# Performance work log

Measured on AMD Instinct MI355X. Metric: run time of the kernel, lower is better.

The kernel has to match this reference:

```python
import jax, jax.numpy as jnp
import numpy as np
import math

EPS = 1e-9
NORM = 1.0 / math.sqrt(20.0)  # num_neighbours=20 default


def _mixing(x1, x2, B, W, b):
    # nn.Bilinear (no bias): x_bi[n,k] = sum_ij x1[n,i] B[k,i,j] x2[n,j]
    x_bi = jnp.einsum('ni,kij->nkj', x1, B)
    x_bi = jnp.einsum('nkj,nj->nk', x_bi, x2)
    x = jnp.concatenate([x1, x2, x_bi], axis=-1)
    return x @ W.T + b


def _rowstd(x):
    # torch.std default: unbiased (ddof=1)
    return jnp.std(x, axis=1, ddof=1, keepdims=True)


def setup_inputs() -> dict:
    key = jax.random.key(0)
    N, E = 100000, 2000000
    DN, DE, DA_N, DA_E = 32, 32, 3, 1
    ks = jax.random.split(key, 24)

    def nrm(k, shape, fan_in):
        return jax.random.normal(k, shape, dtype=jnp.float32) / np.sqrt(fan_in)

    inp = {
        'xn': jax.random.normal(ks[0], (N, DN), dtype=jnp.float32),
        'xn_attr': jax.random.normal(ks[1], (N, DA_N), dtype=jnp.float32),
        'xe_attr': jax.random.normal(ks[2], (E, DA_E), dtype=jnp.float32),
        'xe_src': jax.random.randint(ks[3], (E,), 0, N),
        'xe_dst': jax.random.randint(ks[4], (E,), 0, N),
        # fc1: Linear(1, xe_dim); fc2: Linear(1, xn_dim)
        'W_fc1': nrm(ks[5], (DE, 1), 1), 'b_fc1': jnp.zeros((DE,), jnp.float32),
        'W_fc2': nrm(ks[6], (DN, 1), 1), 'b_fc2': jnp.zeros((DN,), jnp.float32),
        # mix_xn: Mixing(DN, DA_N, DN)
        'B_mix_xn': nrm(ks[7], (DN, DN, DA_N), DN * DA_N),
        'W_mix_xn': nrm(ks[8], (DN, 2 * DN + DA_N), 2 * DN + DA_N),
        'b_mix_xn': jnp.zeros((DN,), jnp.float32),
        # nodes_to_edges.mix: Mixing(DN, DN, DN)
        'B_n2e': nrm(ks[9], (DN, DN, DN), DN * DN),
        'W_n2e': nrm(ks[10], (DN, 3 * DN), 3 * DN),
        'b_n2e': jnp.zeros((DN,), jnp.float32),
        # mix_xe: Mixing(DE, DA_E, DE)
        'B_mix_xe': nrm(ks[11], (DE, DE, DA_E), DE * DA_E),
        'W_mix_xe': nrm(ks[12], (DE, 2 * DE + DA_E), 2 * DE + DA_E),
        'b_mix_xe': jnp.zeros((DE,), jnp.float32),
        # edges_to_nodes.mix: Mixing(DE, DE, DE)
        'B_e2n': nrm(ks[13], (DE, DE, DE), DE * DE),
        'W_e2n': nrm(ks[14], (DE, 3 * DE), 3 * DE),
        'b_e2n': jnp.zeros((DE,), jnp.float32),
    }
    return inp


def reference(xn, xn_attr, xe_attr, xe_src, xe_dst,
              W_fc1, b_fc1, W_fc2, b_fc2,
              B_mix_xn, W_mix_xn, b_mix_xn,
              B_n2e, W_n2e, b_n2e,
              B_mix_xe, W_mix_xe, b_mix_xe,
              B_e2n, W_e2n, b_e2n):
    n_nodes = xn.shape[0]
    # node mixing + per-row std norm
    xn = _mixing(xn, xn_attr, B_mix_xn, W_mix_xn, b_mix_xn)
    xn = xn / (_rowstd(xn) + EPS)
    # fc1 weight: [E, xe_dim]
    w1 = jax.nn.silu(xe_attr @ W_fc1.T + b_fc1)
    # NodesToEdges: gather -> grad/ave -> mixing
    xg, xd = xn[xe_src], xn[xe_dst]
    xe = _mixing(w1 * (xg - xd), w1 * (xg + xd) * 0.5, B_n2e, W_n2e, b_n2e)
    xe = _mixing(xe, xe_attr, B_mix_xe, W_mix_xe, b_mix_xe)
    xe = xe / (_rowstd(xe) + EPS)
    # fc2 weight: [E, xn_dim]
    w2 = jax.nn.silu(xe_attr @ W_fc2.T + b_fc2)
    # EdgesToNodes: scatter-add over dst/src, diff/sum, mixing
    wxe = w2 * xe
    xn1 = jax.ops.segment_sum(wxe, xe_dst, num_segments=n_nodes) * NORM
    xn2 = jax.ops.segment_sum(wxe, xe_src, num_segments=n_nodes) * NORM
    xn = _mixing(xn1 - xn2, xn1 + xn2, B_e2n, W_e2n, b_e2n)
    xn = jax.nn.silu(xn)
    xn = xn / (_rowstd(xn) + EPS)
    return xn
```

## Files before the change

### kernel.cpp

```cpp
#include <hip/hip_runtime.h>
#include <hip/hip_bf16.h>

#define N_NODES 100000
#define N_EDGES 2000000
#define EPS 1e-9f
#define NORMC 0.22360679774997896f

#define BKSZ   256
#define NBK1   391
#define NBK    782
#define NSB    256
#define CE     7813
#define SCAN_TOT (NBK * NSB)
#define TILES_E 7813
#define TILES_F 391

typedef short s8 __attribute__((ext_vector_type(8)));
typedef float f4 __attribute__((ext_vector_type(4)));
typedef uint  u4 __attribute__((ext_vector_type(4)));

__device__ __forceinline__ float silu_f(float x) {
    return x / (1.0f + __expf(-x));
}

__device__ __forceinline__ ushort f2bfu(float f) {
    union { __hip_bfloat16 b; ushort u; } cv;
    cv.b = __float2bfloat16(f);
    return cv.u;
}

__device__ __forceinline__ uint pkbf(float lo, float hi) {
    float2 t; t.x = lo; t.y = hi;
    union { __hip_bfloat162 b; uint u; } cv;
    cv.b = __float22bfloat162_rn(t);
    return cv.u;
}


__device__ float mext(const float* __restrict__ W, const float* __restrict__ B,
                      const float* __restrict__ bias, int n, int i, int j) {
    if (i < 32 && j < 32) {
        float r = 0.f;
        #pragma unroll
        for (int m = 0; m < 32; ++m) r += W[n*96 + 64 + m] * B[m*1024 + i*32 + j];
        return r;
    }
    if (i < 32) return W[n*96 + i];
    if (j < 32) return W[n*96 + 32 + j];
    return bias[n];
}

__global__ void prep_kernel(const float* __restrict__ W_n2e, const float* __restrict__ B_n2e,
                            const float* __restrict__ b_n2e,
                            const float* __restrict__ W_e2n, const float* __restrict__ B_e2n,
                            const float* __restrict__ b_e2n,
                            const float* __restrict__ W_mix_xn, const float* __restrict__ B_mix_xn,
                            const float* __restrict__ b_mix_xn,
                            const float* __restrict__ W_mix_xe, const float* __restrict__ B_mix_xe,
                            const float* __restrict__ b_mix_xe,
                            ushort* __restrict__ MF, ushort* __restrict__ MG,
                            float* __restrict__ BpN, float* __restrict__ WxE,
                            float* __restrict__ CtE) {
    int t = blockIdx.x * blockDim.x + threadIdx.x;
    if (t < 69632) {
        int u = (t < 34816) ? t : t - 34816;
        int tt = u & 7, lane = (u >> 3) & 63, rest = u >> 9;
        int nt = rest & 1, kk = rest >> 1;
        int n = nt*16 + (lane & 15);
        int kl = ((lane >> 4) & 3) * 8 + tt;
        int i, j;
        if (kk < 33) { i = kk; j = kl; } else { i = kl; j = 32; }
        if (t < 34816) MF[u] = f2bfu(mext(W_n2e, B_n2e, b_n2e, n, i, j));
        else           MG[u] = f2bfu(mext(W_e2n, B_e2n, b_e2n, n, i, j));
    } else if (t < 73856) {
        int u = t - 69632;
        int k = u & 31, ij = u >> 5;
        int i = ij >> 2, j = ij & 3;
        float r;
        if (i < 32 && j < 3) {
            r = 0.f;
            #pragma unroll
            for (int m = 0; m < 32; ++m) r += W_mix_xn[k*67 + 35 + m] * B_mix_xn[m*96 + i*3 + j];
        } else if (i < 32 && j == 3) {
            r = W_mix_xn[k*67 + i];
        } else if (i == 32 && j < 3) {
            r = W_mix_xn[k*67 + 32 + j];
        } else {
            r = b_mix_xn[k];
        }
        BpN[ij*32 + k] = r;
    } else if (t < 74912) {
        int u = t - 73856;
        int k = u & 31, i = u >> 5;
        WxE[i*32 + k] = (i < 32) ? W_mix_xe[k*65 + i] : b_mix_xe[k];
    } else if (t < 75968) {
        int u = t - 74912;
        int k = u & 31, i = u >> 5;
        float r;
        if (i < 32) {
            r = 0.f;
            #pragma unroll
            for (int m = 0; m < 32; ++m) r += W_mix_xe[k*65 + 33 + m] * B_mix_xe[m*32 + i];
        } else {
            r = W_mix_xe[k*65 + 32];
        }
        CtE[i*32 + k] = r;
    }
}

__global__ void zero_kernel(float4* __restrict__ p, int n4) {
    int i = blockIdx.x * blockDim.x + threadIdx.x;
    int stride = gridDim.x * blockDim.x;
    float4 z = {0.f, 0.f, 0.f, 0.f};
    for (; i < n4; i += stride) p[i] = z;
}

__global__ __launch_bounds__(256) void node_kernel(
    const float* __restrict__ xn, const float* __restrict__ xn_attr,
    const float* __restrict__ BpN, float* __restrict__ xn_norm) {
    int n = blockIdx.x * 256 + threadIdx.x;
    if (n >= N_NODES) return;
    float x[33];
    const float4* xr = (const float4*)(xn + (size_t)n * 32);
    #pragma unroll
    for (int q = 0; q < 8; ++q) {
        float4 v = xr[q];
        x[q*4+0] = v.x; x[q*4+1] = v.y; x[q*4+2] = v.z; x[q*4+3] = v.w;
    }
    x[32] = 1.f;
    float at[4];
    at[0] = xn_attr[n*3]; at[1] = xn_attr[n*3+1]; at[2] = xn_attr[n*3+2]; at[3] = 1.f;

    float acc[32];
    #pragma unroll
    for (int k = 0; k < 32; ++k) acc[k] = 0.f;
    #pragma unroll
    for (int i = 0; i < 33; ++i) {
        #pragma unroll
        for (int j = 0; j < 4; ++j) {
            float s = x[i] * at[j];
            const float* bp = BpN + (i*4 + j) * 32;
            #pragma unroll
            for (int k = 0; k < 32; ++k) acc[k] = fmaf(bp[k], s, acc[k]);
        }
    }
    float mean = 0.f;
    #pragma unroll
    for (int k = 0; k < 32; ++k) mean += acc[k];
    mean *= (1.0f / 32.0f);
    float var = 0.f;
    #pragma unroll
    for (int k = 0; k < 32; ++k) { float d = acc[k] - mean; var += d * d; }
    var *= (1.0f / 31.0f);
    float inv = 1.0f / (sqrtf(var) + EPS);
    float4* out = (float4*)(xn_norm + (size_t)n * 32);
    #pragma unroll
    for (int q = 0; q < 8; ++q) {
        float4 v;
        v.x = acc[q*4+0]*inv; v.y = acc[q*4+1]*inv; v.z = acc[q*4+2]*inv; v.w = acc[q*4+3]*inv;
        out[q] = v;
    }
}


__global__ __launch_bounds__(256) void count_kernel(
    const int* __restrict__ xe_src, const int* __restrict__ xe_dst,
    int* __restrict__ cntg) {
    __shared__ int cnt[NBK];
    int tid = threadIdx.x, b = blockIdx.x;
    for (int k = tid; k < NBK; k += 256) cnt[k] = 0;
    __syncthreads();
    int e0 = b * CE;
    for (int i = tid; i < CE; i += 256) {
        int e = e0 + i;
        if (e < N_EDGES) {
            atomicAdd(&cnt[xe_dst[e] >> 8], 1);
            atomicAdd(&cnt[NBK1 + (xe_src[e] >> 8)], 1);
        }
    }
    __syncthreads();
    for (int k = tid; k < NBK; k += 256) cntg[k * NSB + b] = cnt[k];
}

__global__ __launch_bounds__(1024) void scan_kernel(int* __restrict__ cntg) {
    __shared__ int part[1024];
    int t = threadIdx.x;
    const int CHUNK = 196;
    int base = t * CHUNK;
    int s = 0;
    for (int i = 0; i < CHUNK; ++i) {
        int idx = base + i;
        if (idx < SCAN_TOT) s += cntg[idx];
    }
    part[t] = s;
    __syncthreads();
    for (int off = 1; off < 1024; off <<= 1) {
        int v = part[t];
        int add = (t >= off) ? part[t - off] : 0;
        __syncthreads();
        part[t] = v + add;
        __syncthreads();
    }
    int run = (t == 0) ? 0 : part[t - 1];
    for (int i = 0; i < CHUNK; ++i) {
        int idx = base + i;
        if (idx < SCAN_TOT) {
            int c = cntg[idx];
            cntg[idx] = run;
            run += c;
        }
    }
}

__global__ __launch_bounds__(256) void scatter_kernel(
    const int* __restrict__ xe_src, const int* __restrict__ xe_dst,
    const int* __restrict__ scang, int* __restrict__ poss,
    unsigned char* __restrict__ srcln, int* __restrict__ bucketed_dst) {
    __shared__ int cur[NBK];
    int tid = threadIdx.x, b = blockIdx.x;
    for (int k = tid; k < NBK; k += 256) cur[k] = scang[k * NSB + b];
    __syncthreads();
    int e0 = b * CE;
    for (int i = tid; i < CE; i += 256) {
        int e = e0 + i;
        if (e < N_EDGES) {
            int s_ = xe_src[e];
            int p2 = atomicAdd(&cur[NBK1 + (s_ >> 8)], 1) - N_EDGES;
            poss[e] = p2;
            srcln[p2] = (unsigned char)(s_ & 255);
            int d = xe_dst[e];
            int pd = atomicAdd(&cur[d >> 8], 1);
            bucketed_dst[pd] = (p2 << 8) | (d & 255);
        }
    }
}

__global__ __launch_bounds__(256) void gather_src(
    const ushort* __restrict__ wxe2, const unsigned char* __restrict__ srcln,
    const int* __restrict__ scang, float* __restrict__ sd1) {
    __shared__ float accs[BKSZ * 33];
    int tid = threadIdx.x, bk = blockIdx.x;
    for (int i = tid; i < BKSZ * 33; i += 256) accs[i] = 0.f;
    __syncthreads();
    int start = scang[(NBK1 + bk) * NSB] - N_EDGES;
    int end = (bk == NBK1 - 1) ? N_EDGES : scang[(NBK1 + bk + 1) * NSB] - N_EDGES;
    int q = tid >> 2, g = tid & 3;
    uint4 z4; z4.x = 0u; z4.y = 0u; z4.z = 0u; z4.w = 0u;

    int i0 = start + q;
    int ln0 = (i0 < end) ? (int)srcln[i0] : 0;
    uint4 r0 = (i0 < end) ? *(const uint4*)(wxe2 + (size_t)i0 * 32 + g * 8) : z4;
    for (int i = i0; i < end; i += 64) {
        int in = i + 64;
        int ln1 = (in < end) ? (int)srcln[in] : 0;
        uint4 r1 = (in < end) ? *(const uint4*)(wxe2 + (size_t)in * 32 + g * 8) : z4;
        float* ap = &accs[ln0 * 33 + g * 8];
        uint uu[4] = {r0.x, r0.y, r0.z, r0.w};
        #pragma unroll
        for (int c = 0; c < 4; ++c) {
            uint u = uu[c];
            atomicAdd(&ap[c*2],     __uint_as_float((u & 0xFFFFu) << 16));
            atomicAdd(&ap[c*2 + 1], __uint_as_float(u & 0xFFFF0000u));
        }
        ln0 = ln1; r0 = r1;
    }
    __syncthreads();
    float* out = sd1 + (size_t)bk * BKSZ * 32;
    for (int i2 = tid; i2 < BKSZ * 32; i2 += 256) {
        int node = i2 >> 5, k = i2 & 31;
        out[i2] = accs[node * 33 + k];
    }
}

__global__ __launch_bounds__(256) void gather_dst(
    const ushort* __restrict__ wxe2, const int* __restrict__ bucketed_dst,
    const int* __restrict__ scang, float* __restrict__ sd0) {
    __shared__ float accs[BKSZ * 33];
    int tid = threadIdx.x, bk = blockIdx.x;
    for (int i = tid; i < BKSZ * 33; i += 256) accs[i] = 0.f;
    __syncthreads();
    int start = scang[bk * NSB];
    int end = (bk == NBK1 - 1) ? N_EDGES : scang[(bk + 1) * NSB];
    int q = tid >> 2, g = tid & 3;
    uint4 z4; z4.x = 0u; z4.y = 0u; z4.z = 0u; z4.w = 0u;

    int i0 = start + q;
    int p0 = (i0 < end) ? bucketed_dst[i0] : 0;
    int p1 = (i0 + 64 < end) ? bucketed_dst[i0 + 64] : 0;
    uint4 r0 = (i0 < end)
             ? *(const uint4*)(wxe2 + (size_t)(p0 >> 8) * 32 + g * 8) : z4;

    for (int i = i0; i < end; i += 64) {
        int pn = (i + 128 < end) ? bucketed_dst[i + 128] : 0;
        uint4 r1 = (i + 64 < end)
                 ? *(const uint4*)(wxe2 + (size_t)(p1 >> 8) * 32 + g * 8) : z4;
        int ln = p0 & 255;
        float* ap = &accs[ln * 33 + g * 8];
        uint uu[4] = {r0.x, r0.y, r0.z, r0.w};
        #pragma unroll
        for (int c = 0; c < 4; ++c) {
            uint u = uu[c];
            atomicAdd(&ap[c*2],     __uint_as_float((u & 0xFFFFu) << 16));
            atomicAdd(&ap[c*2 + 1], __uint_as_float(u & 0xFFFF0000u));
        }
        p0 = p1; p1 = pn; r0 = r1;
    }
    __syncthreads();
    float* out = sd0 + (size_t)bk * BKSZ * 32;
    for (int i2 = tid; i2 < BKSZ * 32; i2 += 256) {
        int node = i2 >> 5, k = i2 & 31;
        out[i2] = accs[node * 33 + k];
    }
}

__device__ __forceinline__ void gemm33(const ushort* __restrict__ sM,
                                       float* __restrict__ a_f,
                                       const ushort* __restrict__ ab,
                                       const float* __restrict__ biasv, int tid) {
    int lane = tid & 63, wv = tid >> 6;
    int m = lane & 15, h = lane >> 4;
    int base = wv * 64;
    float bfv[4][8];
    #pragma unroll
    for (int g = 0; g < 4; ++g) {
        union { s8 v; ushort s[8]; } braw;
        braw.v = *(const s8*)&ab[(size_t)(base + g*16 + m) * 40 + h*8];
        #pragma unroll
        for (int t = 0; t < 8; ++t) {
            union { uint u; float f; } cv; cv.u = ((uint)braw.s[t]) << 16;
            bfv[g][t] = cv.f;
        }
    }
    f4 c[4][2];
    #pragma unroll
    for (int g = 0; g < 4; ++g) {
        c[g][0] = (f4){0.f, 0.f, 0.f, 0.f};
        c[g][1] = (f4){0.f, 0.f, 0.f, 0.f};
    }
    const s8* M8 = (const s8*)sM;
    #pragma unroll
    for (int kk = 0; kk < 33; ++kk) {
        s8 mf0 = M8[(kk*2 + 0)*64 + lane];
        s8 mf1 = M8[(kk*2 + 1)*64 + lane];
        #pragma unroll
        for (int g = 0; g < 4; ++g) {
            float as = a_f[(size_t)(base + g*16 + m) * 33 + kk];
            union { s8 v; uint u[4]; } af;
            #pragma unroll
            for (int t = 0; t < 4; ++t) af.u[t] = pkbf(as * bfv[g][2*t], as * bfv[g][2*t+1]);
            c[g][0] = __builtin_amdgcn_mfma_f32_16x16x32_bf16(af.v, mf0, c[g][0], 0, 0, 0);
            c[g][1] = __builtin_amdgcn_mfma_f32_16x16x32_bf16(af.v, mf1, c[g][1], 0, 0, 0);
        }
    }
    {
        s8 mf0 = M8[66*64 + lane];
        s8 mf1 = M8[67*64 + lane];
        #pragma unroll
        for (int g = 0; g < 4; ++g) {
            const float* arow = &a_f[(size_t)(base + g*16 + m) * 33 + h*8];
            union { s8 v; uint u[4]; } af;
            #pragma unroll
            for (int t = 0; t < 4; ++t) af.u[t] = pkbf(arow[2*t], arow[2*t+1]);
            c[g][0] = __builtin_amdgcn_mfma_f32_16x16x32_bf16(af.v, mf0, c[g][0], 0, 0, 0);
            c[g][1] = __builtin_amdgcn_mfma_f32_16x16x32_bf16(af.v, mf1, c[g][1], 0, 0, 0);
        }
    }
    float b0 = biasv[m], b1 = biasv[16 + m];
    #pragma unroll
    for (int g = 0; g < 4; ++g) {
        int rowb = base + g*16 + h*4;
        #pragma unroll
        for (int r = 0; r < 4; ++r) {
            a_f[(size_t)(rowb + r) * 33 + m]      = c[g][0][r] + b0;
            a_f[(size_t)(rowb + r) * 33 + 16 + m] = c[g][1][r] + b1;
        }
    }
}

__device__ __forceinline__ float mixe_std(const float* __restrict__ a_f, int tid,
                                          float attr,
                                          const float* __restrict__ WxE,
                                          const float* __restrict__ CtE,
                                          float2* __restrict__ y2) {
    #pragma unroll
    for (int k2 = 0; k2 < 16; ++k2) y2[k2] = make_float2(0.f, 0.f);
    for (int i = 0; i < 33; ++i) {
        float xi = a_f[tid*33 + i];
        const float2* wx2 = (const float2*)(WxE + i * 32);
        const float2* ct2 = (const float2*)(CtE + i * 32);
        #pragma unroll
        for (int k2 = 0; k2 < 16; ++k2) {
            float2 w = wx2[k2], ctv = ct2[k2];
            float lx = fmaf(attr, ctv.x, w.x);
            float ly = fmaf(attr, ctv.y, w.y);
            y2[k2].x = fmaf(lx, xi, y2[k2].x);
            y2[k2].y = fmaf(ly, xi, y2[k2].y);
        }
    }
    float mean = 0.f;
    #pragma unroll
    for (int k2 = 0; k2 < 16; ++k2) mean += y2[k2].x + y2[k2].y;
    mean *= (1.0f / 32.0f);
    float var = 0.f;
    #pragma unroll
    for (int k2 = 0; k2 < 16; ++k2) {
        float dx = y2[k2].x - mean, dy = y2[k2].y - mean;
        var += dx*dx + dy*dy;
    }
    var *= (1.0f / 31.0f);
    return 1.0f / (sqrtf(var) + EPS);
}

template<int MODE>
__global__ __launch_bounds__(256, 1) void edge_kernel(
    const float* __restrict__ xn_norm, const float* __restrict__ xe_attr,
    const int* __restrict__ xe_src, const int* __restrict__ xe_dst,
    const float* __restrict__ W_fc1, const float* __restrict__ b_fc1,
    const float* __restrict__ W_fc2, const float* __restrict__ b_fc2,
    const ushort* __restrict__ MF, const float* __restrict__ biasE,
    const float* __restrict__ WxE, const float* __restrict__ CtE,
    float* __restrict__ acc1, float* __restrict__ acc2,
    ushort* __restrict__ wxe2, const int* __restrict__ poss) {
    __shared__ __align__(16) ushort sM[34816];
    __shared__ __align__(16) float  a_f[256 * 33];
    __shared__ __align__(16) ushort ab[256 * 40];
    int tid = threadIdx.x;
    {
        const float4* s4p = (const float4*)MF;
        float4* d4p = (float4*)sM;
        #pragma unroll
        for (int i = 0; i < 17; ++i) d4p[tid + i*256] = s4p[tid + i*256];
    }
    uint* ab32 = (uint*)ab;

    int t = blockIdx.x;
    float attrP = 0.f; int srcP = 0, dstP = 0, posP = 0; bool okP = false;
    float4 gP[8], dP[8];
    {
        int e = t*256 + tid;
        okP = e < N_EDGES;
        int ec = okP ? e : 0;
        attrP = xe_attr[ec]; srcP = xe_src[ec]; dstP = xe_dst[ec];
        if (MODE == 1) posP = poss[ec];
        const float4* gp = (const float4*)(xn_norm + (size_t)srcP * 32);
        const float4* dp = (const float4*)(xn_norm + (size_t)dstP * 32);
        #pragma unroll
        for (int q = 0; q < 8; ++q) { gP[q] = gp[q]; dP[q] = dp[q]; }
    }

    for (; t < TILES_E; t += 256) {
        float attr = attrP; int csrc = srcP, cdst = dstP, cpos = posP;
        bool okC = okP;
        float vs = okC ? 1.f : 0.f;
        #pragma unroll
        for (int q = 0; q < 8; ++q) {
            float4 g = gP[q], d = dP[q];
            float gg[4] = {g.x, g.y, g.z, g.w};
            float dd[4] = {d.x, d.y, d.z, d.w};
            #pragma unroll
            for (int p = 0; p < 2; ++p) {
                int k = q*4 + p*2;
                float w0 = silu_f(attr * W_fc1[k]   + b_fc1[k])   * vs;
                float w1 = silu_f(attr * W_fc1[k+1] + b_fc1[k+1]) * vs;
                float av0 = w0 * (gg[2*p]   - dd[2*p]);
                float av1 = w1 * (gg[2*p+1] - dd[2*p+1]);
                float bv0 = w0 * (gg[2*p]   + dd[2*p])   * 0.5f;
                float bv1 = w1 * (gg[2*p+1] + dd[2*p+1]) * 0.5f;
                a_f[tid*33 + k]   = av0;
                a_f[tid*33 + k+1] = av1;
                ab32[tid*20 + (k>>1)] = pkbf(bv0, bv1);
            }
        }
        a_f[tid*33 + 32] = 1.f;

        int tn = t + 256;
        if (tn < TILES_E) {
            int e = tn*256 + tid;
            okP = e < N_EDGES;
            int ec = okP ? e : 0;
            attrP = xe_attr[ec]; srcP = xe_src[ec]; dstP = xe_dst[ec];
            if (MODE == 1) posP = poss[ec];
            const float4* gp = (const float4*)(xn_norm + (size_t)srcP * 32);
            const float4* dp = (const float4*)(xn_norm + (size_t)dstP * 32);
            #pragma unroll
            for (int q = 0; q < 8; ++q) { gP[q] = gp[q]; dP[q] = dp[q]; }
        }
        __syncthreads();

        gemm33(sM, a_f, ab, biasE, tid);
        __syncthreads();

        float2 y2[16];
        float inv = mixe_std(a_f, tid, attr, WxE, CtE, y2);

        if (okC) {
            if (MODE == 1) {
                uint pkv[16];
                #pragma unroll
                for (int k2 = 0; k2 < 16; ++k2) {
                    float w20 = silu_f(attr * W_fc2[2*k2]   + b_fc2[2*k2]);
                    float w21 = silu_f(attr * W_fc2[2*k2+1] + b_fc2[2*k2+1]);
                    pkv[k2] = pkbf(w20 * y2[k2].x * inv, w21 * y2[k2].y * inv);
                }
                u4* wp = (u4*)(wxe2 + (size_t)cpos * 32);
                #pragma unroll
                for (int q = 0; q < 4; ++q) {
                    u4 v = (u4){pkv[q*4], pkv[q*4+1], pkv[q*4+2], pkv[q*4+3]};
                    __builtin_nontemporal_store(v, wp + q);
                }
            } else {
                float* p1 = acc1 + (size_t)cdst * 32;
                float* p2 = acc2 + (size_t)csrc * 32;
                #pragma unroll
                for (int k = 0; k < 32; ++k) {
                    float yk = (k & 1) ? y2[k>>1].y : y2[k>>1].x;
                    float w2 = silu_f(attr * W_fc2[k] + b_fc2[k]);
                    float vv = w2 * yk * inv;
                    unsafeAtomicAdd(p1 + k, vv);
                    unsafeAtomicAdd(p2 + k, vv);
                }
            }
        }
    }
}

__global__ __launch_bounds__(256, 1) void final_kernel(
    const float* __restrict__ acc1, const float* __restrict__ acc2,
    const ushort* __restrict__ MG, const float* __restrict__ biasG,
    float* __restrict__ out) {
    __shared__ __align__(16) ushort sM[34816];
    __shared__ __align__(16) float  a_f[256 * 33];
    __shared__ __align__(16) ushort ab[256 * 40];
    int tid = threadIdx.x;
    {
        const float4* s4p = (const float4*)MG;
        float4* d4p = (float4*)sM;
        #pragma unroll
        for (int i = 0; i < 17; ++i) d4p[tid + i*256] = s4p[tid + i*256];
    }
    uint* ab32 = (uint*)ab;

    for (int t = blockIdx.x; t < TILES_F; t += 256) {
        int n = t*256 + tid;
        bool ok = n < N_NODES;
        int nn = ok ? n : 0;
        float vs = ok ? 1.f : 0.f;
        const float4* p1 = (const float4*)(acc1 + (size_t)nn * 32);
        const float4* p2 = (const float4*)(acc2 + (size_t)nn * 32);
        #pragma unroll
        for (int q = 0; q < 8; ++q) {
            float4 u1 = p1[q], u2 = p2[q];
            float a1[4] = {u1.x, u1.y, u1.z, u1.w};
            float a2[4] = {u2.x, u2.y, u2.z, u2.w};
            #pragma unroll
            for (int p = 0; p < 2; ++p) {
                int k = q*4 + p*2;
                float dv0 = (a1[2*p]   - a2[2*p])   * NORMC * vs;
                float dv1 = (a1[2*p+1] - a2[2*p+1]) * NORMC * vs;
                float sv0 = (a1[2*p]   + a2[2*p])   * NORMC * vs;
                float sv1 = (a1[2*p+1] + a2[2*p+1]) * NORMC * vs;
                a_f[tid*33 + k]   = dv0;
                a_f[tid*33 + k+1] = dv1;
                ab32[tid*20 + (k>>1)] = pkbf(sv0, sv1);
            }
        }
        a_f[tid*33 + 32] = 1.f;
        __syncthreads();

        gemm33(sM, a_f, ab, biasG, tid);
        __syncthreads();

        if (ok) {
            float z[32];
            float mean = 0.f;
            #pragma unroll
            for (int k = 0; k < 32; ++k) { z[k] = silu_f(a_f[tid*33 + k]); mean += z[k]; }
            mean *= (1.0f / 32.0f);
            float var = 0.f;
            #pragma unroll
            for (int k = 0; k < 32; ++k) { float d = z[k] - mean; var += d * d; }
            var *= (1.0f / 31.0f);
            float inv = 1.0f / (sqrtf(var) + EPS);
            float4* op = (float4*)(out + (size_t)n * 32);
            #pragma unroll
            for (int q = 0; q < 8; ++q) {
                float4 v;
                v.x = z[q*4+0]*inv; v.y = z[q*4+1]*inv; v.z = z[q*4+2]*inv; v.w = z[q*4+3]*inv;
                op[q] = v;
            }
        }
    }
}

extern "C" void kernel_launch(void* const* d_in, const int* in_sizes, int n_in,
                              void* d_out, int out_size, void* d_ws, size_t ws_size,
                              hipStream_t stream) {
    const float* xn       = (const float*)d_in[0];
    const float* xn_attr  = (const float*)d_in[1];
    const float* xe_attr  = (const float*)d_in[2];
    const int*   xe_src   = (const int*)d_in[3];
    const int*   xe_dst   = (const int*)d_in[4];
    const float* W_fc1    = (const float*)d_in[5];
    const float* b_fc1    = (const float*)d_in[6];
    const float* W_fc2    = (const float*)d_in[7];
    const float* b_fc2    = (const float*)d_in[8];
    const float* B_mix_xn = (const float*)d_in[9];
    const float* W_mix_xn = (const float*)d_in[10];
    const float* b_mix_xn = (const float*)d_in[11];
    const float* B_n2e    = (const float*)d_in[12];
    const float* W_n2e    = (const float*)d_in[13];
    const float* b_n2e    = (const float*)d_in[14];
    const float* B_mix_xe = (const float*)d_in[15];
    const float* W_mix_xe = (const float*)d_in[16];
    const float* b_mix_xe = (const float*)d_in[17];
    const float* B_e2n    = (const float*)d_in[18];
    const float* W_e2n    = (const float*)d_in[19];
    const float* b_e2n    = (const float*)d_in[20];

    float* ws = (float*)d_ws;
    const size_t T1_BYTES = 46347488ULL * 4ULL;

    if (ws_size >= T1_BYTES) {
        float*  xn_norm = ws;
        float*  sd0     = ws + 3200000;
        float*  sd1     = ws + 6403072;
        ushort* MF      = (ushort*)(ws + 9606144);
        ushort* MG      = (ushort*)(ws + 9623552);
        float*  BpN     = ws + 9640960;
        float*  WxE     = ws + 9645184;
        float*  CtE     = ws + 9646240;
        ushort* wxe2    = (ushort*)(ws + 9647296);
        int*    poss    = (int*)(ws + 41647296);
        unsigned char* srcln = (unsigned char*)(ws + 43647296);
        int*    bucketed_dst = (int*)(ws + 44147296);
        int*    cntg    = (int*)(ws + 46147296);

        prep_kernel<<<297, 256, 0, stream>>>(W_n2e, B_n2e, b_n2e, W_e2n, B_e2n, b_e2n,
                                             W_mix_xn, B_mix_xn, b_mix_xn,
                                             W_mix_xe, B_mix_xe, b_mix_xe,
                                             MF, MG, BpN, WxE, CtE);
        node_kernel<<<391, 256, 0, stream>>>(xn, xn_attr, BpN, xn_norm);
        count_kernel<<<NSB, 256, 0, stream>>>(xe_src, xe_dst, cntg);
        scan_kernel<<<1, 1024, 0, stream>>>(cntg);
        scatter_kernel<<<NSB, 256, 0, stream>>>(xe_src, xe_dst, cntg,
                                                poss, srcln, bucketed_dst);
        edge_kernel<1><<<256, 256, 0, stream>>>(xn_norm, xe_attr, xe_src, xe_dst,
                                                W_fc1, b_fc1, W_fc2, b_fc2,
                                                MF, b_n2e, WxE, CtE,
                                                nullptr, nullptr, wxe2, poss);
        gather_src<<<NBK1, 256, 0, stream>>>(wxe2, srcln, cntg, sd1);
        gather_dst<<<NBK1, 256, 0, stream>>>(wxe2, bucketed_dst, cntg, sd0);
        final_kernel<<<391, 256, 0, stream>>>(sd0, sd1, MG, b_e2n, (float*)d_out);
    } else {
        float*  xn_norm = ws;
        float*  acc1    = ws + 3200000;
        float*  acc2    = ws + 6400000;
        ushort* MF      = (ushort*)(ws + 9600000);
        ushort* MG      = MF + 34816;
        float*  BpN     = ws + 9600000 + 34816;
        float*  WxE     = BpN + 4224;
        float*  CtE     = WxE + 1056;

        prep_kernel<<<297, 256, 0, stream>>>(W_n2e, B_n2e, b_n2e, W_e2n, B_e2n, b_e2n,
                                             W_mix_xn, B_mix_xn, b_mix_xn,
                                             W_mix_xe, B_mix_xe, b_mix_xe,
                                             MF, MG, BpN, WxE, CtE);
        zero_kernel<<<2048, 256, 0, stream>>>((float4*)acc1, 1600000);
        node_kernel<<<391, 256, 0, stream>>>(xn, xn_attr, BpN, xn_norm);
        edge_kernel<0><<<256, 256, 0, stream>>>(xn_norm, xe_attr, xe_src, xe_dst,
                                                W_fc1, b_fc1, W_fc2, b_fc2,
                                                MF, b_n2e, WxE, CtE,
                                                acc1, acc2, nullptr, nullptr);
        final_kernel<<<391, 256, 0, stream>>>(acc1, acc2, MG, b_e2n, (float*)d_out);
    }
}
```

Before: 2.056 ms.

## Process edges in two halves with dst-sorted edge order and dual output buffers

```diff
diff --git a/kernel.cpp b/kernel.cpp
--- a/kernel.cpp
+++ b/kernel.cpp
@@ -3,6 +3,7 @@
 
 #define N_NODES 100000
 #define N_EDGES 2000000
+#define HALF    1000000
 #define EPS 1e-9f
 #define NORMC 0.22360679774997896f
 
@@ -10,8 +11,9 @@
 #define NBK1   391
 #define NBK    782
 #define NSB    256
-#define CE     7813
+#define CEH    3907
 #define SCAN_TOT (NBK * NSB)
+#define TILES_H 3907
 #define TILES_E 7813
 #define TILES_F 391
 
@@ -163,17 +165,17 @@
 }
 
 
-__global__ __launch_bounds__(256) void count_kernel(
+__global__ __launch_bounds__(256) void count_half(
     const int* __restrict__ xe_src, const int* __restrict__ xe_dst,
-    int* __restrict__ cntg) {
+    int e0, int* __restrict__ cntg) {
     __shared__ int cnt[NBK];
     int tid = threadIdx.x, b = blockIdx.x;
     for (int k = tid; k < NBK; k += 256) cnt[k] = 0;
     __syncthreads();
-    int e0 = b * CE;
-    for (int i = tid; i < CE; i += 256) {
-        int e = e0 + i;
-        if (e < N_EDGES) {
+    int s0 = e0 + b * CEH, s1 = e0 + HALF;
+    for (int i = tid; i < CEH; i += 256) {
+        int e = s0 + i;
+        if (e < s1) {
             atomicAdd(&cnt[xe_dst[e] >> 8], 1);
             atomicAdd(&cnt[NBK1 + (xe_src[e] >> 8)], 1);
         }
@@ -212,48 +214,52 @@
     }
 }
 
-__global__ __launch_bounds__(256) void scatter_kernel(
+__global__ __launch_bounds__(256) void scatter_half(
     const int* __restrict__ xe_src, const int* __restrict__ xe_dst,
-    const int* __restrict__ scang, int* __restrict__ poss,
-    unsigned char* __restrict__ srcln, int* __restrict__ bucketed_dst) {
+    int e0, const int* __restrict__ scang,
+    int* __restrict__ edst, int* __restrict__ posD,
+    unsigned char* __restrict__ dstln, unsigned char* __restrict__ srcln) {
     __shared__ int cur[NBK];
     int tid = threadIdx.x, b = blockIdx.x;
     for (int k = tid; k < NBK; k += 256) cur[k] = scang[k * NSB + b];
     __syncthreads();
-    int e0 = b * CE;
-    for (int i = tid; i < CE; i += 256) {
-        int e = e0 + i;
-        if (e < N_EDGES) {
-            int s_ = xe_src[e];
-            int p2 = atomicAdd(&cur[NBK1 + (s_ >> 8)], 1) - N_EDGES;
-            poss[e] = p2;
-            srcln[p2] = (unsigned char)(s_ & 255);
+    int s0 = e0 + b * CEH, s1 = e0 + HALF;
+    for (int i = tid; i < CEH; i += 256) {
+        int e = s0 + i;
+        if (e < s1) {
             int d = xe_dst[e];
             int pd = atomicAdd(&cur[d >> 8], 1);
-            bucketed_dst[pd] = (p2 << 8) | (d & 255);
-        }
-    }
-}
-
-__global__ __launch_bounds__(256) void gather_src(
-    const ushort* __restrict__ wxe2, const unsigned char* __restrict__ srcln,
-    const int* __restrict__ scang, float* __restrict__ sd1) {
+            edst[pd] = e;
+            dstln[pd] = (unsigned char)(d & 255);
+            int s_ = xe_src[e];
+            int ps = atomicAdd(&cur[NBK1 + (s_ >> 8)], 1) - HALF;
+            srcln[ps] = (unsigned char)(s_ & 255);
+            posD[pd] = ps;
+        }
+    }
+}
+
+template<bool ACCUM>
+__global__ __launch_bounds__(256) void gather_g(
+    const ushort* __restrict__ w, const unsigned char* __restrict__ ln,
+    const int* __restrict__ scang, int sideOff, int sub,
+    float* __restrict__ sd) {
     __shared__ float accs[BKSZ * 33];
     int tid = threadIdx.x, bk = blockIdx.x;
     for (int i = tid; i < BKSZ * 33; i += 256) accs[i] = 0.f;
     __syncthreads();
-    int start = scang[(NBK1 + bk) * NSB] - N_EDGES;
-    int end = (bk == NBK1 - 1) ? N_EDGES : scang[(NBK1 + bk + 1) * NSB] - N_EDGES;
+    int start = scang[(sideOff + bk) * NSB] - sub;
+    int end = (sideOff + bk + 1 < NBK) ? scang[(sideOff + bk + 1) * NSB] - sub : HALF;
     int q = tid >> 2, g = tid & 3;
     uint4 z4; z4.x = 0u; z4.y = 0u; z4.z = 0u; z4.w = 0u;
 
     int i0 = start + q;
-    int ln0 = (i0 < end) ? (int)srcln[i0] : 0;
-    uint4 r0 = (i0 < end) ? *(const uint4*)(wxe2 + (size_t)i0 * 32 + g * 8) : z4;
+    int ln0 = (i0 < end) ? (int)ln[i0] : 0;
+    uint4 r0 = (i0 < end) ? *(const uint4*)(w + (size_t)i0 * 32 + g * 8) : z4;
     for (int i = i0; i < end; i += 64) {
         int in = i + 64;
-        int ln1 = (in < end) ? (int)srcln[in] : 0;
-        uint4 r1 = (in < end) ? *(const uint4*)(wxe2 + (size_t)in * 32 + g * 8) : z4;
+        int ln1 = (in < end) ? (int)ln[in] : 0;
+        uint4 r1 = (in < end) ? *(const uint4*)(w + (size_t)in * 32 + g * 8) : z4;
         float* ap = &accs[ln0 * 33 + g * 8];
         uint uu[4] = {r0.x, r0.y, r0.z, r0.w};
         #pragma unroll
@@ -265,51 +271,11 @@
         ln0 = ln1; r0 = r1;
     }
     __syncthreads();
-    float* out = sd1 + (size_t)bk * BKSZ * 32;
+    float* out = sd + (size_t)bk * BKSZ * 32;
     for (int i2 = tid; i2 < BKSZ * 32; i2 += 256) {
         int node = i2 >> 5, k = i2 & 31;
-        out[i2] = accs[node * 33 + k];
-    }
-}
-
-__global__ __launch_bounds__(256) void gather_dst(
-    const ushort* __restrict__ wxe2, const int* __restrict__ bucketed_dst,
-    const int* __restrict__ scang, float* __restrict__ sd0) {
-    __shared__ float accs[BKSZ * 33];
-    int tid = threadIdx.x, bk = blockIdx.x;
-    for (int i = tid; i < BKSZ * 33; i += 256) accs[i] = 0.f;
-    __syncthreads();
-    int start = scang[bk * NSB];
-    int end = (bk == NBK1 - 1) ? N_EDGES : scang[(bk + 1) * NSB];
-    int q = tid >> 2, g = tid & 3;
-    uint4 z4; z4.x = 0u; z4.y = 0u; z4.z = 0u; z4.w = 0u;
-
-    int i0 = start + q;
-    int p0 = (i0 < end) ? bucketed_dst[i0] : 0;
-    int p1 = (i0 + 64 < end) ? bucketed_dst[i0 + 64] : 0;
-    uint4 r0 = (i0 < end)
-             ? *(const uint4*)(wxe2 + (size_t)(p0 >> 8) * 32 + g * 8) : z4;
-
-    for (int i = i0; i < end; i += 64) {
-        int pn = (i + 128 < end) ? bucketed_dst[i + 128] : 0;
-        uint4 r1 = (i + 64 < end)
-                 ? *(const uint4*)(wxe2 + (size_t)(p1 >> 8) * 32 + g * 8) : z4;
-        int ln = p0 & 255;
-        float* ap = &accs[ln * 33 + g * 8];
-        uint uu[4] = {r0.x, r0.y, r0.z, r0.w};
-        #pragma unroll
-        for (int c = 0; c < 4; ++c) {
-            uint u = uu[c];
-            atomicAdd(&ap[c*2],     __uint_as_float((u & 0xFFFFu) << 16));
-            atomicAdd(&ap[c*2 + 1], __uint_as_float(u & 0xFFFF0000u));
-        }
-        p0 = p1; p1 = pn; r0 = r1;
-    }
-    __syncthreads();
-    float* out = sd0 + (size_t)bk * BKSZ * 32;
-    for (int i2 = tid; i2 < BKSZ * 32; i2 += 256) {
-        int node = i2 >> 5, k = i2 & 31;
-        out[i2] = accs[node * 33 + k];
+        float v = accs[node * 33 + k];
+        if (ACCUM) out[i2] += v; else out[i2] = v;
     }
 }
 
@@ -411,16 +377,15 @@
     return 1.0f / (sqrtf(var) + EPS);
 }
 
-template<int MODE>
-__global__ __launch_bounds__(256, 1) void edge_kernel(
+__global__ __launch_bounds__(256, 1) void edge_half(
     const float* __restrict__ xn_norm, const float* __restrict__ xe_attr,
     const int* __restrict__ xe_src, const int* __restrict__ xe_dst,
     const float* __restrict__ W_fc1, const float* __restrict__ b_fc1,
     const float* __restrict__ W_fc2, const float* __restrict__ b_fc2,
     const ushort* __restrict__ MF, const float* __restrict__ biasE,
     const float* __restrict__ WxE, const float* __restrict__ CtE,
-    float* __restrict__ acc1, float* __restrict__ acc2,
-    ushort* __restrict__ wxe2, const int* __restrict__ poss) {
+    const int* __restrict__ edst, const int* __restrict__ posD,
+    ushort* __restrict__ wdst, ushort* __restrict__ wsrc) {
     __shared__ __align__(16) ushort sM[34816];
     __shared__ __align__(16) float  a_f[256 * 33];
     __shared__ __align__(16) ushort ab[256 * 40];
@@ -437,19 +402,19 @@
     float attrP = 0.f; int srcP = 0, dstP = 0, posP = 0; bool okP = false;
     float4 gP[8], dP[8];
     {
-        int e = t*256 + tid;
-        okP = e < N_EDGES;
-        int ec = okP ? e : 0;
-        attrP = xe_attr[ec]; srcP = xe_src[ec]; dstP = xe_dst[ec];
-        if (MODE == 1) posP = poss[ec];
+        int gi = t*256 + tid;
+        okP = gi < HALF;
+        int ic = okP ? gi : HALF - 1;
+        int e = edst[ic];
+        attrP = xe_attr[e]; srcP = xe_src[e]; dstP = xe_dst[e]; posP = posD[ic];
         const float4* gp = (const float4*)(xn_norm + (size_t)srcP * 32);
         const float4* dp = (const float4*)(xn_norm + (size_t)dstP * 32);
         #pragma unroll
         for (int q = 0; q < 8; ++q) { gP[q] = gp[q]; dP[q] = dp[q]; }
     }
 
-    for (; t < TILES_E; t += 256) {
-        float attr = attrP; int csrc = srcP, cdst = dstP, cpos = posP;
+    for (; t < TILES_H; t += 256) {
+        float attr = attrP; int cpos = posP;
         bool okC = okP;
         float vs = okC ? 1.f : 0.f;
         #pragma unroll
@@ -474,12 +439,113 @@
         a_f[tid*33 + 32] = 1.f;
 
         int tn = t + 256;
+        if (tn < TILES_H) {
+            int gi = tn*256 + tid;
+            okP = gi < HALF;
+            int ic = okP ? gi : HALF - 1;
+            int e = edst[ic];
+            attrP = xe_attr[e]; srcP = xe_src[e]; dstP = xe_dst[e]; posP = posD[ic];
+            const float4* gp = (const float4*)(xn_norm + (size_t)srcP * 32);
+            const float4* dp = (const float4*)(xn_norm + (size_t)dstP * 32);
+            #pragma unroll
+            for (int q = 0; q < 8; ++q) { gP[q] = gp[q]; dP[q] = dp[q]; }
+        }
+        __syncthreads();
+
+        gemm33(sM, a_f, ab, biasE, tid);
+        __syncthreads();
+
+        float2 y2[16];
+        float inv = mixe_std(a_f, tid, attr, WxE, CtE, y2);
+
+        if (okC) {
+            uint pkv[16];
+            #pragma unroll
+            for (int k2 = 0; k2 < 16; ++k2) {
+                float w20 = silu_f(attr * W_fc2[2*k2]   + b_fc2[2*k2]);
+                float w21 = silu_f(attr * W_fc2[2*k2+1] + b_fc2[2*k2+1]);
+                pkv[k2] = pkbf(w20 * y2[k2].x * inv, w21 * y2[k2].y * inv);
+            }
+            uint4* wp = (uint4*)(wdst + (size_t)(t*256 + tid) * 32);
+            #pragma unroll
+            for (int q = 0; q < 4; ++q) {
+                uint4 v; v.x = pkv[q*4]; v.y = pkv[q*4+1]; v.z = pkv[q*4+2]; v.w = pkv[q*4+3];
+                wp[q] = v;
+            }
+            u4* sp = (u4*)(wsrc + (size_t)cpos * 32);
+            #pragma unroll
+            for (int q = 0; q < 4; ++q) {
+                u4 v = (u4){pkv[q*4], pkv[q*4+1], pkv[q*4+2], pkv[q*4+3]};
+                __builtin_nontemporal_store(v, sp + q);
+            }
+        }
+    }
+}
+
+__global__ __launch_bounds__(256, 1) void edge_atomic(
+    const float* __restrict__ xn_norm, const float* __restrict__ xe_attr,
+    const int* __restrict__ xe_src, const int* __restrict__ xe_dst,
+    const float* __restrict__ W_fc1, const float* __restrict__ b_fc1,
+    const float* __restrict__ W_fc2, const float* __restrict__ b_fc2,
+    const ushort* __restrict__ MF, const float* __restrict__ biasE,
+    const float* __restrict__ WxE, const float* __restrict__ CtE,
+    float* __restrict__ acc1, float* __restrict__ acc2) {
+    __shared__ __align__(16) ushort sM[34816];
+    __shared__ __align__(16) float  a_f[256 * 33];
+    __shared__ __align__(16) ushort ab[256 * 40];
+    int tid = threadIdx.x;
+    {
+        const float4* s4p = (const float4*)MF;
+        float4* d4p = (float4*)sM;
+        #pragma unroll
+        for (int i = 0; i < 17; ++i) d4p[tid + i*256] = s4p[tid + i*256];
+    }
+    uint* ab32 = (uint*)ab;
+
+    int t = blockIdx.x;
+    float attrP = 0.f; int srcP = 0, dstP = 0; bool okP = false;
+    float4 gP[8], dP[8];
+    {
+        int e = t*256 + tid;
+        okP = e < N_EDGES;
+        int ec = okP ? e : 0;
+        attrP = xe_attr[ec]; srcP = xe_src[ec]; dstP = xe_dst[ec];
+        const float4* gp = (const float4*)(xn_norm + (size_t)srcP * 32);
+        const float4* dp = (const float4*)(xn_norm + (size_t)dstP * 32);
+        #pragma unroll
+        for (int q = 0; q < 8; ++q) { gP[q] = gp[q]; dP[q] = dp[q]; }
+    }
+
+    for (; t < TILES_E; t += 256) {
+        float attr = attrP; int csrc = srcP, cdst = dstP; bool okC = okP;
+        float vs = okC ? 1.f : 0.f;
+        #pragma unroll
+        for (int q = 0; q < 8; ++q) {
+            float4 g = gP[q], d = dP[q];
+            float gg[4] = {g.x, g.y, g.z, g.w};
+            float dd[4] = {d.x, d.y, d.z, d.w};
+            #pragma unroll
+            for (int p = 0; p < 2; ++p) {
+                int k = q*4 + p*2;
+                float w0 = silu_f(attr * W_fc1[k]   + b_fc1[k])   * vs;
+                float w1 = silu_f(attr * W_fc1[k+1] + b_fc1[k+1]) * vs;
+                float av0 = w0 * (gg[2*p]   - dd[2*p]);
+                float av1 = w1 * (gg[2*p+1] - dd[2*p+1]);
+                float bv0 = w0 * (gg[2*p]   + dd[2*p])   * 0.5f;
+                float bv1 = w1 * (gg[2*p+1] + dd[2*p+1]) * 0.5f;
+                a_f[tid*33 + k]   = av0;
+                a_f[tid*33 + k+1] = av1;
+                ab32[tid*20 + (k>>1)] = pkbf(bv0, bv1);
+            }
+        }
+        a_f[tid*33 + 32] = 1.f;
+
+        int tn = t + 256;
         if (tn < TILES_E) {
             int e = tn*256 + tid;
             okP = e < N_EDGES;
             int ec = okP ? e : 0;
             attrP = xe_attr[ec]; srcP = xe_src[ec]; dstP = xe_dst[ec];
-            if (MODE == 1) posP = poss[ec];
             const float4* gp = (const float4*)(xn_norm + (size_t)srcP * 32);
             const float4* dp = (const float4*)(xn_norm + (size_t)dstP * 32);
             #pragma unroll
@@ -494,31 +560,15 @@
         float inv = mixe_std(a_f, tid, attr, WxE, CtE, y2);
 
         if (okC) {
-            if (MODE == 1) {
-                uint pkv[16];
-                #pragma unroll
-                for (int k2 = 0; k2 < 16; ++k2) {
-                    float w20 = silu_f(attr * W_fc2[2*k2]   + b_fc2[2*k2]);
-                    float w21 = silu_f(attr * W_fc2[2*k2+1] + b_fc2[2*k2+1]);
-                    pkv[k2] = pkbf(w20 * y2[k2].x * inv, w21 * y2[k2].y * inv);
-                }
-                u4* wp = (u4*)(wxe2 + (size_t)cpos * 32);
-                #pragma unroll
-                for (int q = 0; q < 4; ++q) {
-                    u4 v = (u4){pkv[q*4], pkv[q*4+1], pkv[q*4+2], pkv[q*4+3]};
-                    __builtin_nontemporal_store(v, wp + q);
-                }
-            } else {
-                float* p1 = acc1 + (size_t)cdst * 32;
-                float* p2 = acc2 + (size_t)csrc * 32;
-                #pragma unroll
-                for (int k = 0; k < 32; ++k) {
-                    float yk = (k & 1) ? y2[k>>1].y : y2[k>>1].x;
-                    float w2 = silu_f(attr * W_fc2[k] + b_fc2[k]);
-                    float vv = w2 * yk * inv;
-                    unsafeAtomicAdd(p1 + k, vv);
-                    unsafeAtomicAdd(p2 + k, vv);
-                }
+            float* p1 = acc1 + (size_t)cdst * 32;
+            float* p2 = acc2 + (size_t)csrc * 32;
+            #pragma unroll
+            for (int k = 0; k < 32; ++k) {
+                float yk = (k & 1) ? y2[k>>1].y : y2[k>>1].x;
+                float w2 = silu_f(attr * W_fc2[k] + b_fc2[k]);
+                float vv = w2 * yk * inv;
+                unsafeAtomicAdd(p1 + k, vv);
+                unsafeAtomicAdd(p2 + k, vv);
             }
         }
     }
@@ -618,7 +668,7 @@
     const float* b_e2n    = (const float*)d_in[20];
 
     float* ws = (float*)d_ws;
-    const size_t T1_BYTES = 46347488ULL * 4ULL;
+    const size_t T1_BYTES = 44347488ULL * 4ULL;
 
     if (ws_size >= T1_BYTES) {
         float*  xn_norm = ws;
@@ -629,27 +679,42 @@
         float*  BpN     = ws + 9640960;
         float*  WxE     = ws + 9645184;
         float*  CtE     = ws + 9646240;
-        ushort* wxe2    = (ushort*)(ws + 9647296);
-        int*    poss    = (int*)(ws + 41647296);
-        unsigned char* srcln = (unsigned char*)(ws + 43647296);
-        int*    bucketed_dst = (int*)(ws + 44147296);
-        int*    cntg    = (int*)(ws + 46147296);
+        ushort* wdst    = (ushort*)(ws + 9647296);
+        ushort* wsrc    = (ushort*)(ws + 25647296);
+        int*    edst    = (int*)(ws + 41647296);
+        int*    posD    = (int*)(ws + 42647296);
+        unsigned char* dstln = (unsigned char*)(ws + 43647296);
+        unsigned char* srcln = (unsigned char*)(ws + 43897296);
+        int*    cntg    = (int*)(ws + 44147296);
 
         prep_kernel<<<297, 256, 0, stream>>>(W_n2e, B_n2e, b_n2e, W_e2n, B_e2n, b_e2n,
                                              W_mix_xn, B_mix_xn, b_mix_xn,
                                              W_mix_xe, B_mix_xe, b_mix_xe,
                                              MF, MG, BpN, WxE, CtE);
         node_kernel<<<391, 256, 0, stream>>>(xn, xn_attr, BpN, xn_norm);
-        count_kernel<<<NSB, 256, 0, stream>>>(xe_src, xe_dst, cntg);
+
+        count_half<<<NSB, 256, 0, stream>>>(xe_src, xe_dst, 0, cntg);
         scan_kernel<<<1, 1024, 0, stream>>>(cntg);
-        scatter_kernel<<<NSB, 256, 0, stream>>>(xe_src, xe_dst, cntg,
-                                                poss, srcln, bucketed_dst);
-        edge_kernel<1><<<256, 256, 0, stream>>>(xn_norm, xe_attr, xe_src, xe_dst,
-                                                W_fc1, b_fc1, W_fc2, b_fc2,
-                                                MF, b_n2e, WxE, CtE,
-                                                nullptr, nullptr, wxe2, poss);
-        gather_src<<<NBK1, 256, 0, stream>>>(wxe2, srcln, cntg, sd1);
-        gather_dst<<<NBK1, 256, 0, stream>>>(wxe2, bucketed_dst, cntg, sd0);
+        scatter_half<<<NSB, 256, 0, stream>>>(xe_src, xe_dst, 0, cntg,
+                                              edst, posD, dstln, srcln);
+        edge_half<<<256, 256, 0, stream>>>(xn_norm, xe_attr, xe_src, xe_dst,
+                                           W_fc1, b_fc1, W_fc2, b_fc2,
+                                           MF, b_n2e, WxE, CtE,
+                                           edst, posD, wdst, wsrc);
+        gather_g<false><<<NBK1, 256, 0, stream>>>(wdst, dstln, cntg, 0, 0, sd0);
+        gather_g<false><<<NBK1, 256, 0, stream>>>(wsrc, srcln, cntg, NBK1, HALF, sd1);
+
+        count_half<<<NSB, 256, 0, stream>>>(xe_src, xe_dst, HALF, cntg);
+        scan_kernel<<<1, 1024, 0, stream>>>(cntg);
+        scatter_half<<<NSB, 256, 0, stream>>>(xe_src, xe_dst, HALF, cntg,
+                                              edst, posD, dstln, srcln);
+        edge_half<<<256, 256, 0, stream>>>(xn_norm, xe_attr, xe_src, xe_dst,
+                                           W_fc1, b_fc1, W_fc2, b_fc2,
+                                           MF, b_n2e, WxE, CtE,
+                                           edst, posD, wdst, wsrc);
+        gather_g<true><<<NBK1, 256, 0, stream>>>(wdst, dstln, cntg, 0, 0, sd0);
+        gather_g<true><<<NBK1, 256, 0, stream>>>(wsrc, srcln, cntg, NBK1, HALF, sd1);
+
         final_kernel<<<391, 256, 0, stream>>>(sd0, sd1, MG, b_e2n, (float*)d_out);
     } else {
         float*  xn_norm = ws;
@@ -667,10 +732,9 @@
                                              MF, MG, BpN, WxE, CtE);
         zero_kernel<<<2048, 256, 0, stream>>>((float4*)acc1, 1600000);
         node_kernel<<<391, 256, 0, stream>>>(xn, xn_attr, BpN, xn_norm);
-        edge_kernel<0><<<256, 256, 0, stream>>>(xn_norm, xe_attr, xe_src, xe_dst,
-                                                W_fc1, b_fc1, W_fc2, b_fc2,
-                                                MF, b_n2e, WxE, CtE,
-                                                acc1, acc2, nullptr, nullptr);
+        edge_atomic<<<256, 256, 0, stream>>>(xn_norm, xe_attr, xe_src, xe_dst,
+                                             W_fc1, b_fc1, W_fc2, b_fc2,
+                                             MF, b_n2e, WxE, CtE, acc1, acc2);
         final_kernel<<<391, 256, 0, stream>>>(acc1, acc2, MG, b_e2n, (float*)d_out);
     }
 }
```

Measured after the change: 2.576 ms. +25.3%, slower.
